# Performance work log

Measured on AMD Instinct MI355X. Metric: run time of the kernel, lower is better.

The kernel has to match this reference:

```python
import jax, jax.numpy as jnp
import numpy as np

N_CELL = 100_000
N_NET = 100_000
N_PIN = 500_000
N_NN = 200_000
N_PAIR = 500_000
RC, RN, RP = 16, 16, 8   # raw cell/net/pin feats
HC, HN, HP = 64, 64, 8   # hidden cell/net/pin feats


def _seg(x, idx, n):
    return jax.ops.segment_sum(x, idx, num_segments=n)


def _ssp(x):  # DGL ShiftedSoftplus used inside CFConv
    return jax.nn.softplus(x) - jnp.log(2.0)


def _graph_conv(x_src, src, dst, n_src, n_dst, W, b):
    # DGL GraphConv, norm='both': c_src = out_deg^-1/2, c_dst = in_deg^-1/2, degrees clamped to >=1
    ones = jnp.ones(src.shape[0], x_src.dtype)
    cs = jnp.clip(_seg(ones, src, n_src), 1.0) ** -0.5
    cd = jnp.clip(_seg(ones, dst, n_dst), 1.0) ** -0.5
    msg = _seg((x_src * cs[:, None])[src], dst, n_dst) * cd[:, None]
    return msg @ W + b


def setup_inputs() -> dict:
    key = jax.random.key(0)
    ks = jax.random.split(key, 40)
    f = lambda i, s: jax.random.normal(ks[i], s, jnp.float32)
    p = lambda i, s: jax.random.normal(ks[i], s, jnp.float32) * 0.05
    ri = lambda i, s, hi: jax.random.randint(ks[i], s, 0, hi)
    return dict(
        cell_feat=f(0, (N_CELL, RC)),
        net_feat=f(1, (N_NET, RN)),
        pin_feat=f(2, (N_PIN, RP)),
        cell_lin_w=p(3, (RC, HC)), cell_lin_b=p(4, (HC,)),
        net_lin_w=p(5, (RN, HN)), net_lin_b=p(6, (HN,)),
        pin_lin_w=p(7, (RP, HP)), pin_lin_b=p(8, (HP,)),
        pins_w=p(9, (HC, HN)), pins_b=p(10, (HN,)),
        father_w=p(11, (HN, HN)), father_b=p(12, (HN,)),
        son_w=p(13, (HN, HN)), son_b=p(14, (HN,)),
        cf_node_w=p(15, (HN, HC)), cf_node_b=p(16, (HC,)),
        cf_e1_w=p(17, (RP, HC)), cf_e1_b=p(18, (HC,)),
        cf_e2_w=p(19, (HC, HC)), cf_e2_b=p(20, (HC,)),
        cf_out_w=p(21, (HC, HC)), cf_out_b=p(22, (HC,)),
        net_dis_w=p(23, (2 * HN, 1)), net_dis_b=p(24, (1,)),
        net_angle_w=p(25, (2 * HN, 1)), net_angle_b=p(26, (1,)),
        pin_dis_w=p(27, (HC + HP + HN, 1)), pin_dis_b=p(28, (1,)),
        pin_angle_w=p(29, (HC + HP + HN, 1)), pin_angle_b=p(30, (1,)),
        pin_net=ri(31, (N_PIN,), N_NET),
        pin_cell=ri(32, (N_PIN,), N_CELL),
        nn_src=ri(33, (N_NN,), N_NET),
        nn_dst=ri(34, (N_NN,), N_NET),
        net_net_pairs=ri(35, (N_PAIR, 2), N_NET),
    )


def reference(cell_feat, net_feat, pin_feat,
              cell_lin_w, cell_lin_b, net_lin_w, net_lin_b, pin_lin_w, pin_lin_b,
              pins_w, pins_b, father_w, father_b, son_w, son_b,
              cf_node_w, cf_node_b, cf_e1_w, cf_e1_b, cf_e2_w, cf_e2_b, cf_out_w, cf_out_b,
              net_dis_w, net_dis_b, net_angle_w, net_angle_b,
              pin_dis_w, pin_dis_b, pin_angle_w, pin_angle_b,
              pin_net, pin_cell, nn_src, nn_dst, net_net_pairs):
    h_cell = jnp.tanh(cell_feat @ cell_lin_w + cell_lin_b)
    h_net = jnp.tanh(net_feat @ net_lin_w + net_lin_b)
    h_pin = jnp.tanh(pin_feat @ pin_lin_w + pin_lin_b)

    # HeteroGraphConv with aggregate='max' (all relations read the PRE-update h)
    net_pins = _graph_conv(h_cell, pin_cell, pin_net, N_CELL, N_NET, pins_w, pins_b)   # cell->net
    net_fa = _graph_conv(h_net, nn_src, nn_dst, N_NET, N_NET, father_w, father_b)      # net->net
    net_so = _graph_conv(h_net, nn_dst, nn_src, N_NET, N_NET, son_w, son_b)            # reversed
    h_net2 = jnp.maximum(jnp.maximum(net_pins, net_fa), net_so)

    # CFConv net->cell; NOTE: original passes RAW pin_feat as edge feats
    e = _ssp(_ssp(pin_feat @ cf_e1_w + cf_e1_b) @ cf_e2_w + cf_e2_b)   # [P, HC]
    hv = h_net @ cf_node_w + cf_node_b                                  # [Nn, HC]
    h_cell2 = _ssp(_seg(hv[pin_net] * e, pin_cell, N_CELL) @ cf_out_w + cf_out_b)

    # gather-based pairwise readouts
    npair = jnp.concatenate([h_net2[net_net_pairs[:, 0]], h_net2[net_net_pairs[:, 1]]], axis=-1)
    npc = jnp.concatenate([h_net2[pin_net], h_pin, h_cell2[pin_cell]], axis=-1)
    net_dis = jax.nn.softplus(npair @ net_dis_w + net_dis_b)[:, 0]
    net_angle = (npair @ net_angle_w + net_angle_b)[:, 0]
    pin_dis = jax.nn.softplus(npc @ pin_dis_w + pin_dis_b)[:, 0]
    pin_angle = (npc @ pin_angle_w + pin_angle_b)[:, 0]
    return (net_dis, net_angle, pin_dis, pin_angle)
```

## Files before the change

### kernel.cpp

```cpp
#include <hip/hip_runtime.h>
#include <math.h>

#define NCELL 100000
#define NNET  100000
#define NPIN  500000
#define NNN   200000
#define NPAIR 500000
#define NSCAN (4 * NNET)
#define SCAN_BLOCKS ((NSCAN + 1023) / 1024)
#define PART_SZ ((NNET + 7) / 8)

typedef __attribute__((ext_vector_type(8))) short short8;
typedef __attribute__((ext_vector_type(4))) float f32x4;
typedef unsigned short u16;
typedef unsigned int u32;
typedef unsigned long long u64;

__device__ __forceinline__ u16 f2bf(float x) {
    union { float f; u32 u; } v; v.f = x;
    u32 r = (v.u + 0x7FFF + ((v.u >> 16) & 1)) >> 16;
    return (u16)r;
}
__device__ __forceinline__ float bf2f(u16 u) {
    union { u32 u; float f; } v; v.u = ((u32)u) << 16; return v.f;
}
__device__ __forceinline__ u32 cvtpk(float lo, float hi) {
    u32 r;
    asm("v_cvt_pk_bf16_f32 %0, %1, %2" : "=v"(r) : "v"(lo), "v"(hi));
    return r;
}
__device__ __forceinline__ u16 f2bf_fast(float v) {
    return (u16)(cvtpk(v, v) & 0xffffu);
}
__device__ __forceinline__ float plo(u32 h) { return bf2f((u16)(h & 0xffff)); }
__device__ __forceinline__ float phi(u32 h) { return bf2f((u16)(h >> 16)); }

__device__ __forceinline__ float softplusf(float x) {
    return fmaxf(x, 0.f) + __logf(1.f + __expf(-fabsf(x)));
}
__device__ __forceinline__ float sspf(float x) {
    return softplusf(x) - 0.69314718055994530942f;
}
__device__ __forceinline__ float ftanh(float x) {
    float xc = fminf(fmaxf(x, -9.f), 9.f);
    float e = __expf(2.f * xc);
    return (e - 1.f) * __builtin_amdgcn_rcpf(e + 1.f);
}

__device__ __forceinline__ short8 load_bfrag(const float* __restrict__ W,
                                             int kt, int nt, int lane) {
    int k0 = kt * 32 + ((lane >> 4) & 3) * 8;
    int c = nt * 16 + (lane & 15);
    short8 f;
#pragma unroll
    for (int j = 0; j < 8; j++) f[j] = (short)f2bf(W[(k0 + j) * 64 + c]);
    return f;
}

__global__ void k_degrees(const int* __restrict__ pin_cell, const int* __restrict__ pin_net,
                          const int* __restrict__ nn_src, const int* __restrict__ nn_dst,
                          u32* __restrict__ cnt,
                          u32* __restrict__ rankNp, u32* __restrict__ rankC,
                          u32* __restrict__ rankD, u32* __restrict__ rankS) {
    int i = blockIdx.x * blockDim.x + threadIdx.x;
    if (i < NPIN) {
        rankNp[i] = atomicAdd(&cnt[pin_net[i]], 1u);
        rankC[i]  = atomicAdd(&cnt[NNET + pin_cell[i]], 1u);
    }
    if (i < NNN) {
        rankD[i] = atomicAdd(&cnt[2 * NNET + nn_dst[i]], 1u);
        rankS[i] = atomicAdd(&cnt[3 * NNET + nn_src[i]], 1u);
    }
}

__global__ void k_deg_fin(const u32* __restrict__ cnt, float* __restrict__ deg) {
    int i = blockIdx.x * blockDim.x + threadIdx.x;
    if (i < NSCAN) deg[i] = rsqrtf((float)max(cnt[i], 1u));
}

__global__ __launch_bounds__(256) void k_scan1(const u32* __restrict__ in,
                                               u32* __restrict__ out, u32* __restrict__ bsum) {
    __shared__ u32 sc[256];
    int t = threadIdx.x;
    int base = blockIdx.x * 1024 + t * 4;
    u32 v0 = base + 0 < NSCAN ? in[base + 0] : 0;
    u32 v1 = base + 1 < NSCAN ? in[base + 1] : 0;
    u32 v2 = base + 2 < NSCAN ? in[base + 2] : 0;
    u32 v3 = base + 3 < NSCAN ? in[base + 3] : 0;
    u32 s = v0 + v1 + v2 + v3;
    sc[t] = s; __syncthreads();
    for (int off = 1; off < 256; off <<= 1) {
        u32 x = (t >= off) ? sc[t - off] : 0; __syncthreads();
        sc[t] += x; __syncthreads();
    }
    u32 excl = sc[t] - s;
    if (base + 0 < NSCAN) out[base + 0] = excl;
    if (base + 1 < NSCAN) out[base + 1] = excl + v0;
    if (base + 2 < NSCAN) out[base + 2] = excl + v0 + v1;
    if (base + 3 < NSCAN) out[base + 3] = excl + v0 + v1 + v2;
    if (t == 255) bsum[blockIdx.x] = sc[255];
}

__global__ __launch_bounds__(512) void k_scan2(u32* __restrict__ bsum) {
    __shared__ u32 sc[512];
    int t = threadIdx.x;
    u32 v = (t < SCAN_BLOCKS) ? bsum[t] : 0;
    sc[t] = v; __syncthreads();
    for (int off = 1; off < 512; off <<= 1) {
        u32 x = (t >= off) ? sc[t - off] : 0; __syncthreads();
        sc[t] += x; __syncthreads();
    }
    if (t < SCAN_BLOCKS) bsum[t] = sc[t] - v;
}

__global__ __launch_bounds__(256) void k_scan3(u32* __restrict__ S, const u32* __restrict__ bsum) {
    int i = blockIdx.x * blockDim.x + threadIdx.x;
    if (i < NSCAN) S[i] = S[i] + bsum[i >> 10];
    if (i == 0) S[NSCAN] = 2u * NPIN + 2u * NNN;
}

__global__ __launch_bounds__(256) void k_place_part(
    const int* __restrict__ pin_cell, const int* __restrict__ pin_net,
    const int* __restrict__ nn_src, const int* __restrict__ nn_dst,
    const u32* __restrict__ S,
    const u32* __restrict__ rankNp, const u32* __restrict__ rankC,
    const u32* __restrict__ rankD, const u32* __restrict__ rankS,
    u32* __restrict__ colC, u64* __restrict__ colPN,
    u32* __restrict__ colS, u32* __restrict__ colD) {
    int part = blockIdx.x & 7;
    int grp = blockIdx.x >> 3;
    int ngrp = gridDim.x >> 3;
    int lo = part * PART_SZ, hi = lo + PART_SZ;
    int stride = ngrp * 256;
    for (int e = grp * 256 + threadIdx.x; e < NPIN; e += stride) {
        int n = pin_net[e], c = pin_cell[e];
        if (n >= lo && n < hi)
            colC[S[n] + rankNp[e]] = (u32)c;
        if (c >= lo && c < hi)
            colPN[S[NNET + c] + rankC[e] - NPIN] = (u64)(u32)e | ((u64)(u32)n << 32);
    }
    for (int i = grp * 256 + threadIdx.x; i < NNN; i += stride) {
        int s = nn_src[i], d = nn_dst[i];
        if (d >= lo && d < hi)
            colS[S[2 * NNET + d] + rankD[i] - 2u * NPIN] = (u32)s;
        if (s >= lo && s < hi)
            colD[S[3 * NNET + s] + rankS[i] - (2u * NPIN + NNN)] = (u32)d;
    }
}

__global__ __launch_bounds__(256) void k_lin16_all(
    const float* __restrict__ cf, const float* __restrict__ nf,
    const float* __restrict__ Wc, const float* __restrict__ bc,
    const float* __restrict__ Wn, const float* __restrict__ bn,
    const float* __restrict__ rC,
    u16* __restrict__ h_cell, u16* __restrict__ h_net) {
    int tid = threadIdx.x, lane = tid & 63, w = tid >> 6;
    float wc[16], wn[16];
#pragma unroll
    for (int k = 0; k < 16; k++) { wc[k] = Wc[k * 64 + lane]; wn[k] = Wn[k * 64 + lane]; }
    float bC = bc[lane], bN = bn[lane];
    int wave = blockIdx.x * 4 + w, nw = gridDim.x * 4;
    for (int r = wave; r < NCELL; r += nw) {
        const float4* ip = (const float4*)(cf + (size_t)r * 16);
        float4 a = ip[0], bv = ip[1], c = ip[2], d = ip[3];
        float acc = bC;
        acc = fmaf(a.x, wc[0], acc);  acc = fmaf(a.y, wc[1], acc);
        acc = fmaf(a.z, wc[2], acc);  acc = fmaf(a.w, wc[3], acc);
        acc = fmaf(bv.x, wc[4], acc); acc = fmaf(bv.y, wc[5], acc);
        acc = fmaf(bv.z, wc[6], acc); acc = fmaf(bv.w, wc[7], acc);
        acc = fmaf(c.x, wc[8], acc);  acc = fmaf(c.y, wc[9], acc);
        acc = fmaf(c.z, wc[10], acc); acc = fmaf(c.w, wc[11], acc);
        acc = fmaf(d.x, wc[12], acc); acc = fmaf(d.y, wc[13], acc);
        acc = fmaf(d.z, wc[14], acc); acc = fmaf(d.w, wc[15], acc);
        float v = ftanh(acc) * rC[r];
        float vp = __shfl_xor(v, 1, 64);
        if (!(lane & 1))
            *(u32*)(h_cell + (size_t)r * 64 + lane) = cvtpk(v, vp);
    }
    for (int r = wave; r < NNET; r += nw) {
        const float4* ip = (const float4*)(nf + (size_t)r * 16);
        float4 a = ip[0], bv = ip[1], c = ip[2], d = ip[3];
        float acc = bN;
        acc = fmaf(a.x, wn[0], acc);  acc = fmaf(a.y, wn[1], acc);
        acc = fmaf(a.z, wn[2], acc);  acc = fmaf(a.w, wn[3], acc);
        acc = fmaf(bv.x, wn[4], acc); acc = fmaf(bv.y, wn[5], acc);
        acc = fmaf(bv.z, wn[6], acc); acc = fmaf(bv.w, wn[7], acc);
        acc = fmaf(c.x, wn[8], acc);  acc = fmaf(c.y, wn[9], acc);
        acc = fmaf(c.z, wn[10], acc); acc = fmaf(c.w, wn[11], acc);
        acc = fmaf(d.x, wn[12], acc); acc = fmaf(d.y, wn[13], acc);
        acc = fmaf(d.z, wn[14], acc); acc = fmaf(d.w, wn[15], acc);
        float v = ftanh(acc);
        float vp = __shfl_xor(v, 1, 64);
        if (!(lane & 1))
            *(u32*)(h_net + (size_t)r * 64 + lane) = cvtpk(v, vp);
    }
}

__global__ __launch_bounds__(256) void k_gatherP(
    const u32* __restrict__ S, const u32* __restrict__ colC,
    const u16* __restrict__ h_cell, u16* __restrict__ accP) {
    int l32 = threadIdx.x & 31, off2 = l32 * 2;
    int slot = blockIdx.x * 8 + (threadIdx.x >> 5), ns = gridDim.x * 8;
    for (int n = slot; n < NNET; n += ns) {
        u32 b0 = S[n], b1 = S[n + 1];
        float fa = 0.f, fb = 0.f, ga = 0.f, gb = 0.f;
        u32 k = b0;
        for (; k + 1 < b1; k += 2) {
            u32 c0 = colC[k], c1 = colC[k + 1];
            u32 h0 = *(const u32*)(h_cell + (size_t)c0 * 64 + off2);
            u32 h1 = *(const u32*)(h_cell + (size_t)c1 * 64 + off2);
            fa += plo(h0); fb += phi(h0);
            ga += plo(h1); gb += phi(h1);
        }
        if (k < b1) {
            u32 c0 = colC[k];
            u32 h0 = *(const u32*)(h_cell + (size_t)c0 * 64 + off2);
            fa += plo(h0); fb += phi(h0);
        }
        *(u32*)(accP + (size_t)n * 64 + off2) = cvtpk(fa + ga, fb + gb);
    }
}

__global__ __launch_bounds__(256) void k_gatherFS(
    const u32* __restrict__ S, const u32* __restrict__ colS, const u32* __restrict__ colD,
    const u16* __restrict__ h_net, const float* __restrict__ rDv, const float* __restrict__ rSv,
    u16* __restrict__ accF, u16* __restrict__ accS) {
    int l32 = threadIdx.x & 31, off2 = l32 * 2;
    int slot = blockIdx.x * 8 + (threadIdx.x >> 5), ns = gridDim.x * 8;
    for (int r = slot; r < 2 * NNET; r += ns) {
        if (r < NNET) {
            int d = r;
            u32 b0 = S[2 * NNET + d] - 2u * NPIN, b1 = S[2 * NNET + d + 1] - 2u * NPIN;
            float fa = 0.f, fb = 0.f, ga = 0.f, gb = 0.f;
            u32 k = b0;
            for (; k + 1 < b1; k += 2) {
                u32 s0 = colS[k], s1 = colS[k + 1];
                float c0 = rSv[s0], c1 = rSv[s1];
                u32 h0 = *(const u32*)(h_net + (size_t)s0 * 64 + off2);
                u32 h1 = *(const u32*)(h_net + (size_t)s1 * 64 + off2);
                fa = fmaf(plo(h0), c0, fa); fb = fmaf(phi(h0), c0, fb);
                ga = fmaf(plo(h1), c1, ga); gb = fmaf(phi(h1), c1, gb);
            }
            if (k < b1) {
                u32 s0 = colS[k];
                float c0 = rSv[s0];
                u32 h0 = *(const u32*)(h_net + (size_t)s0 * 64 + off2);
                fa = fmaf(plo(h0), c0, fa); fb = fmaf(phi(h0), c0, fb);
            }
            *(u32*)(accF + (size_t)d * 64 + off2) = cvtpk(fa + ga, fb + gb);
        } else {
            int s = r - NNET;
            u32 b0 = S[3 * NNET + s] - (2u * NPIN + NNN), b1 = S[3 * NNET + s + 1] - (2u * NPIN + NNN);
            float fa = 0.f, fb = 0.f, ga = 0.f, gb = 0.f;
            u32 k = b0;
            for (; k + 1 < b1; k += 2) {
                u32 d0 = colD[k], d1 = colD[k + 1];
                float c0 = rDv[d0], c1 = rDv[d1];
                u32 h0 = *(const u32*)(h_net + (size_t)d0 * 64 + off2);
                u32 h1 = *(const u32*)(h_net + (size_t)d1 * 64 + off2);
                fa = fmaf(plo(h0), c0, fa); fb = fmaf(phi(h0), c0, fb);
                ga = fmaf(plo(h1), c1, ga); gb = fmaf(phi(h1), c1, gb);
            }
            if (k < b1) {
                u32 d0 = colD[k];
                float c0 = rDv[d0];
                u32 h0 = *(const u32*)(h_net + (size_t)d0 * 64 + off2);
                fa = fmaf(plo(h0), c0, fa); fb = fmaf(phi(h0), c0, fb);
            }
            *(u32*)(accS + (size_t)s * 64 + off2) = cvtpk(fa + ga, fb + gb);
        }
    }
}

__global__ __launch_bounds__(256) void k_gatherCell(
    const u32* __restrict__ S, const u64* __restrict__ colPN,
    const u16* __restrict__ etab, const u16* __restrict__ hv, u16* __restrict__ acc) {
    int l32 = threadIdx.x & 31, off2 = l32 * 2;
    int slot = blockIdx.x * 8 + (threadIdx.x >> 5), ns = gridDim.x * 8;
    for (int c = slot; c < NCELL; c += ns) {
        u32 b0 = S[NNET + c] - NPIN, b1 = S[NNET + c + 1] - NPIN;
        float fa = 0.f, fb = 0.f, ga = 0.f, gb = 0.f;
        u32 k = b0;
        for (; k + 1 < b1; k += 2) {
            u32 n0 = (u32)(colPN[k] >> 32), n1 = (u32)(colPN[k + 1] >> 32);
            u32 e0 = *(const u32*)(etab + (size_t)k * 64 + off2);
            u32 e1 = *(const u32*)(etab + (size_t)(k + 1) * 64 + off2);
            u32 h0 = *(const u32*)(hv + (size_t)n0 * 64 + off2);
            u32 h1 = *(const u32*)(hv + (size_t)n1 * 64 + off2);
            fa = fmaf(plo(e0), plo(h0), fa); fb = fmaf(phi(e0), phi(h0), fb);
            ga = fmaf(plo(e1), plo(h1), ga); gb = fmaf(phi(e1), phi(h1), gb);
        }
        if (k < b1) {
            u32 n0 = (u32)(colPN[k] >> 32);
            u32 e0 = *(const u32*)(etab + (size_t)k * 64 + off2);
            u32 h0 = *(const u32*)(hv + (size_t)n0 * 64 + off2);
            fa = fmaf(plo(e0), plo(h0), fa); fb = fmaf(phi(e0), phi(h0), fb);
        }
        *(u32*)(acc + (size_t)c * 64 + off2) = cvtpk(fa + ga, fb + gb);
    }
}

__global__ __launch_bounds__(256, 2) void k_combine3(
// ... 56 lines not shown
#pragma unroll
                    for (int r = 0; r < 4; r++)
                        res[nt][r] = fmaxf(res[nt][r], sa[r] * acc[r] + bias[rel][nt]);
                }
            }
        }
#pragma unroll
        for (int r = 0; r < 4; r++) {
            float a0 = 0.f, a1 = 0.f, a2 = 0.f, a3 = 0.f, a4 = 0.f, a5 = 0.f;
#pragma unroll
            for (int nt = 0; nt < 4; nt++) {
                float v = res[nt][r];
                a0 = fmaf(v, wt[0][nt], a0);
                a1 = fmaf(v, wt[1][nt], a1);
                a2 = fmaf(v, wt[2][nt], a2);
                a3 = fmaf(v, wt[3][nt], a3);
                a4 = fmaf(v, wt[4][nt], a4);
                a5 = fmaf(v, wt[5][nt], a5);
            }
#pragma unroll
            for (int off = 1; off < 16; off <<= 1) {
                a0 += __shfl_xor(a0, off, 64);
                a1 += __shfl_xor(a1, off, 64);
                a2 += __shfl_xor(a2, off, 64);
                a3 += __shfl_xor(a3, off, 64);
                a4 += __shfl_xor(a4, off, 64);
                a5 += __shfl_xor(a5, off, 64);
            }
            if (l15 == 0) {
                float* tp = ntab + (size_t)(R + g * 4 + r) * 8;
                *(float2*)tp = float2{a0, a1};
                *(float2*)(tp + 2) = float2{a2, a3};
                *(float2*)(tp + 4) = float2{a4, a5};
            }
        }
    }
}

__global__ __launch_bounds__(256, 4) void k_mm64hv(
    const u16* __restrict__ in, const float* __restrict__ W,
    const float* __restrict__ b, u16* __restrict__ out, int n) {
    int tid = threadIdx.x, lane = tid & 63, w = tid >> 6;
    int l15 = lane & 15, g = (lane >> 4) & 3;
    short8 Bf[2][4];
    float bias[4];
#pragma unroll
    for (int kt = 0; kt < 2; kt++)
#pragma unroll
        for (int nt = 0; nt < 4; nt++) Bf[kt][nt] = load_bfrag(W, kt, nt, lane);
#pragma unroll
    for (int nt = 0; nt < 4; nt++) bias[nt] = b[nt * 16 + l15];
    int wave = blockIdx.x * 4 + w, nwave = gridDim.x * 4;
    int ntile = n >> 4;
    f32x4 z = {0.f, 0.f, 0.f, 0.f};
    for (int t = wave; t < ntile; t += nwave) {
        int R = t << 4;
        const u16* rb = in + (size_t)(R + l15) * 64;
        short8 a0 = *(const short8*)(rb + g * 8);
        short8 a1 = *(const short8*)(rb + 32 + g * 8);
#pragma unroll
        for (int nt = 0; nt < 4; nt++) {
            f32x4 acc = __builtin_amdgcn_mfma_f32_16x16x32_bf16(a0, Bf[0][nt], z, 0, 0, 0);
            acc = __builtin_amdgcn_mfma_f32_16x16x32_bf16(a1, Bf[1][nt], acc, 0, 0, 0);
#pragma unroll
            for (int r = 0; r < 4; r++) {
                float v = acc[r] + bias[nt];
                float vp = __shfl_xor(v, 1, 64);
                if (!(lane & 1))
                    *(u32*)(out + (size_t)(R + g * 4 + r) * 64 + nt * 16 + l15) = cvtpk(v, vp);
            }
        }
    }
}

__global__ __launch_bounds__(256, 4) void k_emlp(
    const float* __restrict__ pin_feat, const u64* __restrict__ colPN,
    const float* __restrict__ E1, const float* __restrict__ b1,
    const float* __restrict__ E2, const float* __restrict__ b2,
    u16* __restrict__ etab) {
    __shared__ __align__(16) u16 sm[4][1024];
    int tid = threadIdx.x, lane = tid & 63, w = tid >> 6;
    int l15 = lane & 15, g = (lane >> 4) & 3;
    short8 B1[4];
#pragma unroll
    for (int nt = 0; nt < 4; nt++) {
        short8 f = {0, 0, 0, 0, 0, 0, 0, 0};
        if (lane < 16) {
            int c = nt * 16 + l15;
#pragma unroll
            for (int j = 0; j < 8; j++) f[j] = (short)f2bf(E1[j * 64 + c]);
        }
        B1[nt] = f;
    }
    short8 B2[2][4];
#pragma unroll
    for (int kt = 0; kt < 2; kt++)
#pragma unroll
        for (int nt = 0; nt < 4; nt++) B2[kt][nt] = load_bfrag(E2, kt, nt, lane);
    float bb1[4], bb2[4];
#pragma unroll
    for (int nt = 0; nt < 4; nt++) {
        bb1[nt] = b1[nt * 16 + l15];
        bb2[nt] = b2[nt * 16 + l15];
    }
    int wave = blockIdx.x * 4 + w, nwave = gridDim.x * 4;
    const int ntile = NPIN >> 4;
    f32x4 z = {0.f, 0.f, 0.f, 0.f};
    for (int t = wave; t < ntile; t += nwave) {
        int P = t << 4;
        short8 a1 = {0, 0, 0, 0, 0, 0, 0, 0};
        if (lane < 16) {
            u32 p = (u32)colPN[P + lane];
            const float4* q = (const float4*)(pin_feat + (size_t)p * 8);
            float4 u0 = q[0], u1 = q[1];
            u32 w01 = cvtpk(u0.x, u0.y), w23 = cvtpk(u0.z, u0.w);
            u32 w45 = cvtpk(u1.x, u1.y), w67 = cvtpk(u1.z, u1.w);
            a1[0] = (short)(w01 & 0xffff); a1[1] = (short)(w01 >> 16);
            a1[2] = (short)(w23 & 0xffff); a1[3] = (short)(w23 >> 16);
            a1[4] = (short)(w45 & 0xffff); a1[5] = (short)(w45 >> 16);
            a1[6] = (short)(w67 & 0xffff); a1[7] = (short)(w67 >> 16);
        }
#pragma unroll
        for (int nt = 0; nt < 4; nt++) {
            f32x4 c1 = __builtin_amdgcn_mfma_f32_16x16x32_bf16(a1, B1[nt], z, 0, 0, 0);
#pragma unroll
            for (int r = 0; r < 4; r++) {
                int row = g * 4 + r;
                int col = nt * 16 + l15;
                sm[w][row * 64 + (col ^ ((row & 7) << 3))] = f2bf_fast(sspf(c1[r] + bb1[nt]));
            }
        }
        short8 a2[2];
#pragma unroll
        for (int kt = 0; kt < 2; kt++) {
            int idx = l15 * 64 + ((kt * 32 + g * 8) ^ ((l15 & 7) << 3));
            a2[kt] = *(const short8*)&sm[w][idx];
        }
#pragma unroll
        for (int nt = 0; nt < 4; nt++) {
            f32x4 e = __builtin_amdgcn_mfma_f32_16x16x32_bf16(a2[0], B2[0][nt], z, 0, 0, 0);
            e = __builtin_amdgcn_mfma_f32_16x16x32_bf16(a2[1], B2[1][nt], e, 0, 0, 0);
#pragma unroll
            for (int r = 0; r < 4; r++) {
                float v = sspf(e[r] + bb2[nt]);
                float vp = __shfl_xor(v, 1, 64);
                if (!(lane & 1))
                    *(u32*)(etab + (size_t)(P + g * 4 + r) * 64 + nt * 16 + l15) = cvtpk(v, vp);
            }
        }
    }
}

__global__ __launch_bounds__(256, 3) void k_mm64c(
    const u16* __restrict__ in, const float* __restrict__ W, const float* __restrict__ b,
    const float* __restrict__ pdw, const float* __restrict__ paw,
    float* __restrict__ ctab, int n) {
    int tid = threadIdx.x, lane = tid & 63, w = tid >> 6;
    int l15 = lane & 15, g = (lane >> 4) & 3;
    short8 Bf[2][4];
    float bias[4], wdv[4], wav[4];
#pragma unroll
    for (int kt = 0; kt < 2; kt++)
#pragma unroll
        for (int nt = 0; nt < 4; nt++) Bf[kt][nt] = load_bfrag(W, kt, nt, lane);
#pragma unroll
    for (int nt = 0; nt < 4; nt++) {
        int c = nt * 16 + l15;
        bias[nt] = b[c];
        wdv[nt] = pdw[72 + c];
        wav[nt] = paw[72 + c];
    }
    int wave = blockIdx.x * 4 + w, nwave = gridDim.x * 4;
    int ntile = n >> 4;
    f32x4 z = {0.f, 0.f, 0.f, 0.f};
    for (int t = wave; t < ntile; t += nwave) {
        int R = t << 4;
        const u16* rb = in + (size_t)(R + l15) * 64;
        short8 a0 = *(const short8*)(rb + g * 8);
        short8 a1 = *(const short8*)(rb + 32 + g * 8);
        float sd[4] = {0.f, 0.f, 0.f, 0.f}, sa[4] = {0.f, 0.f, 0.f, 0.f};
// ... 80 lines not shown
    const float* father_w = (const float*)d_in[11];
    const float* father_b = (const float*)d_in[12];
    const float* son_w    = (const float*)d_in[13];
    const float* son_b    = (const float*)d_in[14];
    const float* cf_node_w = (const float*)d_in[15];
    const float* cf_node_b = (const float*)d_in[16];
    const float* cf_e1_w  = (const float*)d_in[17];
    const float* cf_e1_b  = (const float*)d_in[18];
    const float* cf_e2_w  = (const float*)d_in[19];
    const float* cf_e2_b  = (const float*)d_in[20];
    const float* cf_out_w = (const float*)d_in[21];
    const float* cf_out_b = (const float*)d_in[22];
    const float* net_dis_w   = (const float*)d_in[23];
    const float* net_dis_b   = (const float*)d_in[24];
    const float* net_angle_w = (const float*)d_in[25];
    const float* net_angle_b = (const float*)d_in[26];
    const float* pin_dis_w   = (const float*)d_in[27];
    const float* pin_dis_b   = (const float*)d_in[28];
    const float* pin_angle_w = (const float*)d_in[29];
    const float* pin_angle_b = (const float*)d_in[30];
    const int* pin_net = (const int*)d_in[31];
    const int* pin_cell = (const int*)d_in[32];
    const int* nn_src = (const int*)d_in[33];
    const int* nn_dst = (const int*)d_in[34];
    const int* pairs = (const int*)d_in[35];

    u16* ws16 = (u16*)d_ws;
    const size_t SZ = (size_t)NNET * 64;
    u16* h_cell   = ws16;
    u16* acc_cell = ws16;
    u16* h_net    = ws16 + SZ;
    u16* accP     = ws16 + 2 * SZ;
    u16* accF     = ws16 + 3 * SZ;
    u16* hv       = ws16 + 3 * SZ;
    u16* accS     = ws16 + 4 * SZ;
    u16* etab     = ws16 + 5 * SZ;
    u32* tail = (u32*)(ws16 + 10 * SZ);
    u32* cnt    = tail;
    u32* Sarr   = cnt + NSCAN;
    u32* rankNp = Sarr + NSCAN + 2;
    u32* rankC  = rankNp + NPIN;
    u32* rankD  = rankC + NPIN;
    u32* rankS  = rankD + NNN;
    u32* colC   = rankS + NNN;
    u32* colS   = colC + NPIN;
    u32* colD   = colS + NNN;
    u64* colPN  = (u64*)(colD + NNN);
    u32* bsum   = (u32*)(colPN + NPIN);
    float* deg  = (float*)(bsum + 512);
    float* rNp = deg;
    float* rC  = deg + NNET;
    float* rD  = deg + 2 * NNET;
    float* rS  = deg + 3 * NNET;
    float* ntab = deg + NSCAN;
    float* ctab = ntab + (size_t)NNET * 8;

    hipMemsetAsync(cnt, 0, NSCAN * sizeof(u32), stream);

    k_degrees<<<(NPIN + 255) / 256, 256, 0, stream>>>(pin_cell, pin_net, nn_src, nn_dst,
                                                      cnt, rankNp, rankC, rankD, rankS);
    k_deg_fin<<<(NSCAN + 255) / 256, 256, 0, stream>>>(cnt, deg);

    k_scan1<<<SCAN_BLOCKS, 256, 0, stream>>>(cnt, Sarr, bsum);
    k_scan2<<<1, 512, 0, stream>>>(bsum);
    k_scan3<<<(NSCAN + 255) / 256, 256, 0, stream>>>(Sarr, bsum);
    k_place_part<<<2048, 256, 0, stream>>>(pin_cell, pin_net, nn_src, nn_dst,
                                           Sarr, rankNp, rankC, rankD, rankS,
                                           colC, colPN, colS, colD);

    k_lin16_all<<<2048, 256, 0, stream>>>(cell_feat, net_feat,
                                          cell_lin_w, cell_lin_b, net_lin_w, net_lin_b,
                                          rC, h_cell, h_net);

    k_gatherP<<<2048, 256, 0, stream>>>(Sarr, colC, h_cell, accP);
    k_gatherFS<<<2048, 256, 0, stream>>>(Sarr, colS, colD, h_net, rD, rS, accF, accS);

    k_combine3<<<512, 256, 0, stream>>>(accP, pins_w, pins_b,
                                        accF, father_w, father_b,
                                        accS, son_w, son_b,
                                        rNp, rD, rS,
                                        net_dis_w, net_angle_w, pin_dis_w, pin_angle_w,
                                        ntab, NNET);

    k_mm64hv<<<1024, 256, 0, stream>>>(h_net, cf_node_w, cf_node_b, hv, NNET);

    k_emlp<<<2048, 256, 0, stream>>>(pin_feat, colPN, cf_e1_w, cf_e1_b, cf_e2_w, cf_e2_b, etab);

    k_gatherCell<<<2048, 256, 0, stream>>>(Sarr, colPN, etab, hv, acc_cell);

    k_mm64c<<<512, 256, 0, stream>>>(acc_cell, cf_out_w, cf_out_b,
                                     pin_dis_w, pin_angle_w, ctab, NCELL);

    float* out = (float*)d_out;
    k_readout<<<(NPAIR + NPIN + 255) / 256, 256, 0, stream>>>(
        pairs, pin_feat, pin_net, pin_cell, ntab, ctab,
        pin_lin_w, pin_lin_b, pin_dis_w, pin_angle_w,
        net_dis_b, net_angle_b, pin_dis_b, pin_angle_b, out);
}
```

Baseline: 310.0 us.

## Merge independent stages into block-partitioned fused kernels to cut launches

Independent stages now share one launch each, with block ranges assigning roles. Degree counting and the input linear layers run together in one kernel. The edge MLP, hv projection, pin gather and father/son gathers run together in a second kernel. The degree rsqrt moves into the scan kernel, and the rC scaling moves from the cell linear into the pin gather, since rC is not ready when the fused first kernel runs. hv gets its own workspace slot so it no longer aliases accF. The aim is fewer launches, less idle tail between stages and concurrent use of the GPU by heterogeneous work. The cost is fixed role splits that may be imbalanced and a fused kernel with higher register pressure.

```diff
diff --git a/kernel.cpp b/kernel.cpp
--- a/kernel.cpp
+++ b/kernel.cpp
@@ -10,6 +10,13 @@
 #define SCAN_BLOCKS ((NSCAN + 1023) / 1024)
 #define PART_SZ ((NNET + 7) / 8)
 
+#define GA_DEG 1024
+#define GA_LIN 1024
+#define GB_EMLP 1024
+#define GB_HV   256
+#define GB_GP   384
+#define GB_GFS  384
+
 typedef __attribute__((ext_vector_type(8))) short short8;
 typedef __attribute__((ext_vector_type(4))) float f32x4;
 typedef unsigned short u16;
@@ -57,29 +64,73 @@
     return f;
 }
 
-__global__ void k_degrees(const int* __restrict__ pin_cell, const int* __restrict__ pin_net,
-                          const int* __restrict__ nn_src, const int* __restrict__ nn_dst,
-                          u32* __restrict__ cnt,
-                          u32* __restrict__ rankNp, u32* __restrict__ rankC,
-                          u32* __restrict__ rankD, u32* __restrict__ rankS) {
-    int i = blockIdx.x * blockDim.x + threadIdx.x;
-    if (i < NPIN) {
-        rankNp[i] = atomicAdd(&cnt[pin_net[i]], 1u);
-        rankC[i]  = atomicAdd(&cnt[NNET + pin_cell[i]], 1u);
-    }
-    if (i < NNN) {
-        rankD[i] = atomicAdd(&cnt[2 * NNET + nn_dst[i]], 1u);
-        rankS[i] = atomicAdd(&cnt[3 * NNET + nn_src[i]], 1u);
-    }
-}
-
-__global__ void k_deg_fin(const u32* __restrict__ cnt, float* __restrict__ deg) {
-    int i = blockIdx.x * blockDim.x + threadIdx.x;
-    if (i < NSCAN) deg[i] = rsqrtf((float)max(cnt[i], 1u));
+__global__ __launch_bounds__(256) void k_fusedA(
+    const int* __restrict__ pin_cell, const int* __restrict__ pin_net,
+    const int* __restrict__ nn_src, const int* __restrict__ nn_dst,
+    u32* __restrict__ cnt,
+    u32* __restrict__ rankNp, u32* __restrict__ rankC,
+    u32* __restrict__ rankD, u32* __restrict__ rankS,
+    const float* __restrict__ cf, const float* __restrict__ nf,
+    const float* __restrict__ Wc, const float* __restrict__ bc,
+    const float* __restrict__ Wn, const float* __restrict__ bn,
+    u16* __restrict__ h_cell, u16* __restrict__ h_net) {
+    if (blockIdx.x < GA_DEG) {
+        int stride = GA_DEG * 256;
+        for (int i = blockIdx.x * 256 + threadIdx.x; i < NPIN; i += stride) {
+            rankNp[i] = atomicAdd(&cnt[pin_net[i]], 1u);
+            rankC[i]  = atomicAdd(&cnt[NNET + pin_cell[i]], 1u);
+        }
+        for (int i = blockIdx.x * 256 + threadIdx.x; i < NNN; i += stride) {
+            rankD[i] = atomicAdd(&cnt[2 * NNET + nn_dst[i]], 1u);
+            rankS[i] = atomicAdd(&cnt[3 * NNET + nn_src[i]], 1u);
+        }
+    } else {
+        int tid = threadIdx.x, lane = tid & 63, w = tid >> 6;
+        float wc[16], wn[16];
+#pragma unroll
+        for (int k = 0; k < 16; k++) { wc[k] = Wc[k * 64 + lane]; wn[k] = Wn[k * 64 + lane]; }
+        float bC = bc[lane], bN = bn[lane];
+        int wave = (blockIdx.x - GA_DEG) * 4 + w, nw = GA_LIN * 4;
+        for (int r = wave; r < NCELL; r += nw) {
+            const float4* ip = (const float4*)(cf + (size_t)r * 16);
+            float4 a = ip[0], bv = ip[1], c = ip[2], d = ip[3];
+            float acc = bC;
+            acc = fmaf(a.x, wc[0], acc);  acc = fmaf(a.y, wc[1], acc);
+            acc = fmaf(a.z, wc[2], acc);  acc = fmaf(a.w, wc[3], acc);
+            acc = fmaf(bv.x, wc[4], acc); acc = fmaf(bv.y, wc[5], acc);
+            acc = fmaf(bv.z, wc[6], acc); acc = fmaf(bv.w, wc[7], acc);
+            acc = fmaf(c.x, wc[8], acc);  acc = fmaf(c.y, wc[9], acc);
+            acc = fmaf(c.z, wc[10], acc); acc = fmaf(c.w, wc[11], acc);
+            acc = fmaf(d.x, wc[12], acc); acc = fmaf(d.y, wc[13], acc);
+            acc = fmaf(d.z, wc[14], acc); acc = fmaf(d.w, wc[15], acc);
+            float v = ftanh(acc);
+            float vp = __shfl_xor(v, 1, 64);
+            if (!(lane & 1))
+                *(u32*)(h_cell + (size_t)r * 64 + lane) = cvtpk(v, vp);
+        }
+        for (int r = wave; r < NNET; r += nw) {
+            const float4* ip = (const float4*)(nf + (size_t)r * 16);
+            float4 a = ip[0], bv = ip[1], c = ip[2], d = ip[3];
+            float acc = bN;
+            acc = fmaf(a.x, wn[0], acc);  acc = fmaf(a.y, wn[1], acc);
+            acc = fmaf(a.z, wn[2], acc);  acc = fmaf(a.w, wn[3], acc);
+            acc = fmaf(bv.x, wn[4], acc); acc = fmaf(bv.y, wn[5], acc);
+            acc = fmaf(bv.z, wn[6], acc); acc = fmaf(bv.w, wn[7], acc);
+            acc = fmaf(c.x, wn[8], acc);  acc = fmaf(c.y, wn[9], acc);
+            acc = fmaf(c.z, wn[10], acc); acc = fmaf(c.w, wn[11], acc);
+            acc = fmaf(d.x, wn[12], acc); acc = fmaf(d.y, wn[13], acc);
+            acc = fmaf(d.z, wn[14], acc); acc = fmaf(d.w, wn[15], acc);
+            float v = ftanh(acc);
+            float vp = __shfl_xor(v, 1, 64);
+            if (!(lane & 1))
+                *(u32*)(h_net + (size_t)r * 64 + lane) = cvtpk(v, vp);
+        }
+    }
 }
 
 __global__ __launch_bounds__(256) void k_scan1(const u32* __restrict__ in,
-                                               u32* __restrict__ out, u32* __restrict__ bsum) {
+                                               u32* __restrict__ out, u32* __restrict__ bsum,
+                                               float* __restrict__ deg) {
     __shared__ u32 sc[256];
     int t = threadIdx.x;
     int base = blockIdx.x * 1024 + t * 4;
@@ -87,6 +138,10 @@
     u32 v1 = base + 1 < NSCAN ? in[base + 1] : 0;
     u32 v2 = base + 2 < NSCAN ? in[base + 2] : 0;
     u32 v3 = base + 3 < NSCAN ? in[base + 3] : 0;
+    if (base + 0 < NSCAN) deg[base + 0] = rsqrtf((float)max(v0, 1u));
+    if (base + 1 < NSCAN) deg[base + 1] = rsqrtf((float)max(v1, 1u));
+    if (base + 2 < NSCAN) deg[base + 2] = rsqrtf((float)max(v2, 1u));
+    if (base + 3 < NSCAN) deg[base + 3] = rsqrtf((float)max(v3, 1u));
     u32 s = v0 + v1 + v2 + v3;
     sc[t] = s; __syncthreads();
     for (int off = 1; off < 256; off <<= 1) {
@@ -148,126 +203,188 @@
     }
 }
 
-__global__ __launch_bounds__(256) void k_lin16_all(
-    const float* __restrict__ cf, const float* __restrict__ nf,
-    const float* __restrict__ Wc, const float* __restrict__ bc,
-    const float* __restrict__ Wn, const float* __restrict__ bn,
-    const float* __restrict__ rC,
-    u16* __restrict__ h_cell, u16* __restrict__ h_net) {
+__global__ __launch_bounds__(256, 4) void k_fusedB(
+    const float* __restrict__ pin_feat, const u64* __restrict__ colPN,
+    const float* __restrict__ E1, const float* __restrict__ b1,
+    const float* __restrict__ E2, const float* __restrict__ b2,
+    u16* __restrict__ etab,
+    const u16* __restrict__ h_net, const float* __restrict__ Whv,
+    const float* __restrict__ bhv, u16* __restrict__ hv,
+    const u32* __restrict__ S, const u32* __restrict__ colC,
+    const u16* __restrict__ h_cell, const float* __restrict__ rCv,
+    u16* __restrict__ accP,
+    const u32* __restrict__ colS, const u32* __restrict__ colD,
+    const float* __restrict__ rDv, const float* __restrict__ rSv,
+    u16* __restrict__ accF, u16* __restrict__ accS) {
+    __shared__ __align__(16) u16 sm[4][1024];
     int tid = threadIdx.x, lane = tid & 63, w = tid >> 6;
-    float wc[16], wn[16];
-#pragma unroll
-    for (int k = 0; k < 16; k++) { wc[k] = Wc[k * 64 + lane]; wn[k] = Wn[k * 64 + lane]; }
-    float bC = bc[lane], bN = bn[lane];
-    int wave = blockIdx.x * 4 + w, nw = gridDim.x * 4;
-    for (int r = wave; r < NCELL; r += nw) {
-        const float4* ip = (const float4*)(cf + (size_t)r * 16);
-        float4 a = ip[0], bv = ip[1], c = ip[2], d = ip[3];
-        float acc = bC;
-        acc = fmaf(a.x, wc[0], acc);  acc = fmaf(a.y, wc[1], acc);
-        acc = fmaf(a.z, wc[2], acc);  acc = fmaf(a.w, wc[3], acc);
-        acc = fmaf(bv.x, wc[4], acc); acc = fmaf(bv.y, wc[5], acc);
-        acc = fmaf(bv.z, wc[6], acc); acc = fmaf(bv.w, wc[7], acc);
-        acc = fmaf(c.x, wc[8], acc);  acc = fmaf(c.y, wc[9], acc);
-        acc = fmaf(c.z, wc[10], acc); acc = fmaf(c.w, wc[11], acc);
-        acc = fmaf(d.x, wc[12], acc); acc = fmaf(d.y, wc[13], acc);
-        acc = fmaf(d.z, wc[14], acc); acc = fmaf(d.w, wc[15], acc);
-        float v = ftanh(acc) * rC[r];
-        float vp = __shfl_xor(v, 1, 64);
-        if (!(lane & 1))
-            *(u32*)(h_cell + (size_t)r * 64 + lane) = cvtpk(v, vp);
-    }
-    for (int r = wave; r < NNET; r += nw) {
-        const float4* ip = (const float4*)(nf + (size_t)r * 16);
-        float4 a = ip[0], bv = ip[1], c = ip[2], d = ip[3];
-        float acc = bN;
-        acc = fmaf(a.x, wn[0], acc);  acc = fmaf(a.y, wn[1], acc);
-        acc = fmaf(a.z, wn[2], acc);  acc = fmaf(a.w, wn[3], acc);
-        acc = fmaf(bv.x, wn[4], acc); acc = fmaf(bv.y, wn[5], acc);
-        acc = fmaf(bv.z, wn[6], acc); acc = fmaf(bv.w, wn[7], acc);
-        acc = fmaf(c.x, wn[8], acc);  acc = fmaf(c.y, wn[9], acc);
-        acc = fmaf(c.z, wn[10], acc); acc = fmaf(c.w, wn[11], acc);
-        acc = fmaf(d.x, wn[12], acc); acc = fmaf(d.y, wn[13], acc);
-        acc = fmaf(d.z, wn[14], acc); acc = fmaf(d.w, wn[15], acc);
-        float v = ftanh(acc);
-        float vp = __shfl_xor(v, 1, 64);
-        if (!(lane & 1))
-            *(u32*)(h_net + (size_t)r * 64 + lane) = cvtpk(v, vp);
-    }
-}
-
-__global__ __launch_bounds__(256) void k_gatherP(
-    const u32* __restrict__ S, const u32* __restrict__ colC,
-    const u16* __restrict__ h_cell, u16* __restrict__ accP) {
-    int l32 = threadIdx.x & 31, off2 = l32 * 2;
-    int slot = blockIdx.x * 8 + (threadIdx.x >> 5), ns = gridDim.x * 8;
-    for (int n = slot; n < NNET; n += ns) {
-        u32 b0 = S[n], b1 = S[n + 1];
-        float fa = 0.f, fb = 0.f, ga = 0.f, gb = 0.f;
-        u32 k = b0;
-        for (; k + 1 < b1; k += 2) {
-            u32 c0 = colC[k], c1 = colC[k + 1];
-            u32 h0 = *(const u32*)(h_cell + (size_t)c0 * 64 + off2);
-            u32 h1 = *(const u32*)(h_cell + (size_t)c1 * 64 + off2);
-            fa += plo(h0); fb += phi(h0);
-            ga += plo(h1); gb += phi(h1);
-        }
-        if (k < b1) {
-            u32 c0 = colC[k];
-            u32 h0 = *(const u32*)(h_cell + (size_t)c0 * 64 + off2);
-            fa += plo(h0); fb += phi(h0);
-        }
-        *(u32*)(accP + (size_t)n * 64 + off2) = cvtpk(fa + ga, fb + gb);
-    }
-}
-
-__global__ __launch_bounds__(256) void k_gatherFS(
-    const u32* __restrict__ S, const u32* __restrict__ colS, const u32* __restrict__ colD,
-    const u16* __restrict__ h_net, const float* __restrict__ rDv, const float* __restrict__ rSv,
-    u16* __restrict__ accF, u16* __restrict__ accS) {
-    int l32 = threadIdx.x & 31, off2 = l32 * 2;
-    int slot = blockIdx.x * 8 + (threadIdx.x >> 5), ns = gridDim.x * 8;
-    for (int r = slot; r < 2 * NNET; r += ns) {
-        if (r < NNET) {
-            int d = r;
-            u32 b0 = S[2 * NNET + d] - 2u * NPIN, b1 = S[2 * NNET + d + 1] - 2u * NPIN;
+    int l15 = lane & 15, g = (lane >> 4) & 3;
+    f32x4 z = {0.f, 0.f, 0.f, 0.f};
+    if (blockIdx.x < GB_EMLP) {
+        short8 B1[4];
+#pragma unroll
+        for (int nt = 0; nt < 4; nt++) {
+            short8 f = {0, 0, 0, 0, 0, 0, 0, 0};
+            if (lane < 16) {
+                int c = nt * 16 + l15;
+#pragma unroll
+                for (int j = 0; j < 8; j++) f[j] = (short)f2bf(E1[j * 64 + c]);
+            }
+            B1[nt] = f;
+        }
+        short8 B2[2][4];
+#pragma unroll
+        for (int kt = 0; kt < 2; kt++)
+#pragma unroll
+            for (int nt = 0; nt < 4; nt++) B2[kt][nt] = load_bfrag(E2, kt, nt, lane);
+        float bb1[4], bb2[4];
+#pragma unroll
+        for (int nt = 0; nt < 4; nt++) {
+            bb1[nt] = b1[nt * 16 + l15];
+            bb2[nt] = b2[nt * 16 + l15];
+        }
+        int wave = blockIdx.x * 4 + w, nwave = GB_EMLP * 4;
+        const int ntile = NPIN >> 4;
+        for (int t = wave; t < ntile; t += nwave) {
+            int P = t << 4;
+            short8 a1 = {0, 0, 0, 0, 0, 0, 0, 0};
+            if (lane < 16) {
+                u32 p = (u32)colPN[P + lane];
+                const float4* q = (const float4*)(pin_feat + (size_t)p * 8);
+                float4 u0 = q[0], u1 = q[1];
+                u32 w01 = cvtpk(u0.x, u0.y), w23 = cvtpk(u0.z, u0.w);
+                u32 w45 = cvtpk(u1.x, u1.y), w67 = cvtpk(u1.z, u1.w);
+                a1[0] = (short)(w01 & 0xffff); a1[1] = (short)(w01 >> 16);
+                a1[2] = (short)(w23 & 0xffff); a1[3] = (short)(w23 >> 16);
+                a1[4] = (short)(w45 & 0xffff); a1[5] = (short)(w45 >> 16);
+                a1[6] = (short)(w67 & 0xffff); a1[7] = (short)(w67 >> 16);
+            }
+#pragma unroll
+            for (int nt = 0; nt < 4; nt++) {
+                f32x4 c1 = __builtin_amdgcn_mfma_f32_16x16x32_bf16(a1, B1[nt], z, 0, 0, 0);
+#pragma unroll
+                for (int r = 0; r < 4; r++) {
+                    int row = g * 4 + r;
+                    int col = nt * 16 + l15;
+                    sm[w][row * 64 + (col ^ ((row & 7) << 3))] = f2bf_fast(sspf(c1[r] + bb1[nt]));
+                }
+            }
+            short8 a2[2];
+#pragma unroll
+            for (int kt = 0; kt < 2; kt++) {
+                int idx = l15 * 64 + ((kt * 32 + g * 8) ^ ((l15 & 7) << 3));
+                a2[kt] = *(const short8*)&sm[w][idx];
+            }
+#pragma unroll
+            for (int nt = 0; nt < 4; nt++) {
+                f32x4 e = __builtin_amdgcn_mfma_f32_16x16x32_bf16(a2[0], B2[0][nt], z, 0, 0, 0);
+                e = __builtin_amdgcn_mfma_f32_16x16x32_bf16(a2[1], B2[1][nt], e, 0, 0, 0);
+#pragma unroll
+                for (int r = 0; r < 4; r++) {
+                    float v = sspf(e[r] + bb2[nt]);
+                    float vp = __shfl_xor(v, 1, 64);
+                    if (!(lane & 1))
+                        *(u32*)(etab + (size_t)(P + g * 4 + r) * 64 + nt * 16 + l15) = cvtpk(v, vp);
+                }
+            }
+        }
+    } else if (blockIdx.x < GB_EMLP + GB_HV) {
+        short8 Bf[2][4];
+        float bias[4];
+#pragma unroll
+        for (int kt = 0; kt < 2; kt++)
+#pragma unroll
+            for (int nt = 0; nt < 4; nt++) Bf[kt][nt] = load_bfrag(Whv, kt, nt, lane);
+#pragma unroll
+        for (int nt = 0; nt < 4; nt++) bias[nt] = bhv[nt * 16 + l15];
+        int wave = (blockIdx.x - GB_EMLP) * 4 + w, nwave = GB_HV * 4;
+        int ntile = NNET >> 4;
+        for (int t = wave; t < ntile; t += nwave) {
+            int R = t << 4;
+            const u16* rb = h_net + (size_t)(R + l15) * 64;
+            short8 a0 = *(const short8*)(rb + g * 8);
+            short8 a1 = *(const short8*)(rb + 32 + g * 8);
+#pragma unroll
+            for (int nt = 0; nt < 4; nt++) {
+                f32x4 acc = __builtin_amdgcn_mfma_f32_16x16x32_bf16(a0, Bf[0][nt], z, 0, 0, 0);
+                acc = __builtin_amdgcn_mfma_f32_16x16x32_bf16(a1, Bf[1][nt], acc, 0, 0, 0);
+#pragma unroll
+                for (int r = 0; r < 4; r++) {
+                    float v = acc[r] + bias[nt];
+                    float vp = __shfl_xor(v, 1, 64);
+                    if (!(lane & 1))
+                        *(u32*)(hv + (size_t)(R + g * 4 + r) * 64 + nt * 16 + l15) = cvtpk(v, vp);
+                }
+            }
+        }
+    } else if (blockIdx.x < GB_EMLP + GB_HV + GB_GP) {
+        int l32 = tid & 31, off2 = l32 * 2;
+        int slot = (blockIdx.x - GB_EMLP - GB_HV) * 8 + (tid >> 5), ns = GB_GP * 8;
+        for (int n = slot; n < NNET; n += ns) {
+            u32 b0 = S[n], b1 = S[n + 1];
             float fa = 0.f, fb = 0.f, ga = 0.f, gb = 0.f;
             u32 k = b0;
             for (; k + 1 < b1; k += 2) {
-                u32 s0 = colS[k], s1 = colS[k + 1];
-                float c0 = rSv[s0], c1 = rSv[s1];
-                u32 h0 = *(const u32*)(h_net + (size_t)s0 * 64 + off2);
-                u32 h1 = *(const u32*)(h_net + (size_t)s1 * 64 + off2);
-                fa = fmaf(plo(h0), c0, fa); fb = fmaf(phi(h0), c0, fb);
-                ga = fmaf(plo(h1), c1, ga); gb = fmaf(phi(h1), c1, gb);
+                u32 c0 = colC[k], c1 = colC[k + 1];
+                float r0 = rCv[c0], r1 = rCv[c1];
+                u32 h0 = *(const u32*)(h_cell + (size_t)c0 * 64 + off2);
+                u32 h1 = *(const u32*)(h_cell + (size_t)c1 * 64 + off2);
+                fa = fmaf(plo(h0), r0, fa); fb = fmaf(phi(h0), r0, fb);
+                ga = fmaf(plo(h1), r1, ga); gb = fmaf(phi(h1), r1, gb);
             }
             if (k < b1) {
-                u32 s0 = colS[k];
-                float c0 = rSv[s0];
-                u32 h0 = *(const u32*)(h_net + (size_t)s0 * 64 + off2);
-                fa = fmaf(plo(h0), c0, fa); fb = fmaf(phi(h0), c0, fb);
-            }
-            *(u32*)(accF + (size_t)d * 64 + off2) = cvtpk(fa + ga, fb + gb);
-        } else {
-            int s = r - NNET;
-            u32 b0 = S[3 * NNET + s] - (2u * NPIN + NNN), b1 = S[3 * NNET + s + 1] - (2u * NPIN + NNN);
-            float fa = 0.f, fb = 0.f, ga = 0.f, gb = 0.f;
-            u32 k = b0;
-            for (; k + 1 < b1; k += 2) {
-                u32 d0 = colD[k], d1 = colD[k + 1];
-                float c0 = rDv[d0], c1 = rDv[d1];
-                u32 h0 = *(const u32*)(h_net + (size_t)d0 * 64 + off2);
-                u32 h1 = *(const u32*)(h_net + (size_t)d1 * 64 + off2);
-                fa = fmaf(plo(h0), c0, fa); fb = fmaf(phi(h0), c0, fb);
-                ga = fmaf(plo(h1), c1, ga); gb = fmaf(phi(h1), c1, gb);
-            }
-            if (k < b1) {
-                u32 d0 = colD[k];
-                float c0 = rDv[d0];
-                u32 h0 = *(const u32*)(h_net + (size_t)d0 * 64 + off2);
-                fa = fmaf(plo(h0), c0, fa); fb = fmaf(phi(h0), c0, fb);
-            }
-            *(u32*)(accS + (size_t)s * 64 + off2) = cvtpk(fa + ga, fb + gb);
+                u32 c0 = colC[k];
+                float r0 = rCv[c0];
+                u32 h0 = *(const u32*)(h_cell + (size_t)c0 * 64 + off2);
+                fa = fmaf(plo(h0), r0, fa); fb = fmaf(phi(h0), r0, fb);
+            }
+            *(u32*)(accP + (size_t)n * 64 + off2) = cvtpk(fa + ga, fb + gb);
+        }
+    } else {
+        int l32 = tid & 31, off2 = l32 * 2;
+        int slot = (blockIdx.x - GB_EMLP - GB_HV - GB_GP) * 8 + (tid >> 5), ns = GB_GFS * 8;
+        for (int r = slot; r < 2 * NNET; r += ns) {
+            if (r < NNET) {
+                int d = r;
+                u32 b0 = S[2 * NNET + d] - 2u * NPIN, b1 = S[2 * NNET + d + 1] - 2u * NPIN;
+                float fa = 0.f, fb = 0.f, ga = 0.f, gb = 0.f;
+                u32 k = b0;
+                for (; k + 1 < b1; k += 2) {
+                    u32 s0 = colS[k], s1 = colS[k + 1];
+                    float c0 = rSv[s0], c1 = rSv[s1];
+                    u32 h0 = *(const u32*)(h_net + (size_t)s0 * 64 + off2);
+                    u32 h1 = *(const u32*)(h_net + (size_t)s1 * 64 + off2);
+                    fa = fmaf(plo(h0), c0, fa); fb = fmaf(phi(h0), c0, fb);
+                    ga = fmaf(plo(h1), c1, ga); gb = fmaf(phi(h1), c1, gb);
+                }
+                if (k < b1) {
+                    u32 s0 = colS[k];
+                    float c0 = rSv[s0];
+                    u32 h0 = *(const u32*)(h_net + (size_t)s0 * 64 + off2);
+                    fa = fmaf(plo(h0), c0, fa); fb = fmaf(phi(h0), c0, fb);
+                }
+                *(u32*)(accF + (size_t)d * 64 + off2) = cvtpk(fa + ga, fb + gb);
+            } else {
+                int s = r - NNET;
+                u32 b0 = S[3 * NNET + s] - (2u * NPIN + NNN), b1 = S[3 * NNET + s + 1] - (2u * NPIN + NNN);
+                float fa = 0.f, fb = 0.f, ga = 0.f, gb = 0.f;
+                u32 k = b0;
+                for (; k + 1 < b1; k += 2) {
+                    u32 d0 = colD[k], d1 = colD[k + 1];
+                    float c0 = rDv[d0], c1 = rDv[d1];
+                    u32 h0 = *(const u32*)(h_net + (size_t)d0 * 64 + off2);
+                    u32 h1 = *(const u32*)(h_net + (size_t)d1 * 64 + off2);
+                    fa = fmaf(plo(h0), c0, fa); fb = fmaf(phi(h0), c0, fb);
+                    ga = fmaf(plo(h1), c1, ga); gb = fmaf(phi(h1), c1, gb);
+                }
+                if (k < b1) {
+                    u32 d0 = colD[k];
+                    float c0 = rDv[d0];
+                    u32 h0 = *(const u32*)(h_net + (size_t)d0 * 64 + off2);
+                    fa = fmaf(plo(h0), c0, fa); fb = fmaf(phi(h0), c0, fb);
+                }
+                *(u32*)(accS + (size_t)s * 64 + off2) = cvtpk(fa + ga, fb + gb);
+            }
         }
     }
 }
@@ -390,120 +507,6 @@
                 *(float2*)tp = float2{a0, a1};
                 *(float2*)(tp + 2) = float2{a2, a3};
                 *(float2*)(tp + 4) = float2{a4, a5};
-            }
-        }
-    }
-}
-
-__global__ __launch_bounds__(256, 4) void k_mm64hv(
-    const u16* __restrict__ in, const float* __restrict__ W,
-    const float* __restrict__ b, u16* __restrict__ out, int n) {
-    int tid = threadIdx.x, lane = tid & 63, w = tid >> 6;
-    int l15 = lane & 15, g = (lane >> 4) & 3;
-    short8 Bf[2][4];
-    float bias[4];
-#pragma unroll
-    for (int kt = 0; kt < 2; kt++)
-#pragma unroll
-        for (int nt = 0; nt < 4; nt++) Bf[kt][nt] = load_bfrag(W, kt, nt, lane);
-#pragma unroll
-    for (int nt = 0; nt < 4; nt++) bias[nt] = b[nt * 16 + l15];
-    int wave = blockIdx.x * 4 + w, nwave = gridDim.x * 4;
-    int ntile = n >> 4;
-    f32x4 z = {0.f, 0.f, 0.f, 0.f};
-    for (int t = wave; t < ntile; t += nwave) {
-        int R = t << 4;
-        const u16* rb = in + (size_t)(R + l15) * 64;
-        short8 a0 = *(const short8*)(rb + g * 8);
-        short8 a1 = *(const short8*)(rb + 32 + g * 8);
-#pragma unroll
-        for (int nt = 0; nt < 4; nt++) {
-            f32x4 acc = __builtin_amdgcn_mfma_f32_16x16x32_bf16(a0, Bf[0][nt], z, 0, 0, 0);
-            acc = __builtin_amdgcn_mfma_f32_16x16x32_bf16(a1, Bf[1][nt], acc, 0, 0, 0);
-#pragma unroll
-            for (int r = 0; r < 4; r++) {
-                float v = acc[r] + bias[nt];
-                float vp = __shfl_xor(v, 1, 64);
-                if (!(lane & 1))
-                    *(u32*)(out + (size_t)(R + g * 4 + r) * 64 + nt * 16 + l15) = cvtpk(v, vp);
-            }
-        }
-    }
-}
-
-__global__ __launch_bounds__(256, 4) void k_emlp(
-    const float* __restrict__ pin_feat, const u64* __restrict__ colPN,
-    const float* __restrict__ E1, const float* __restrict__ b1,
-    const float* __restrict__ E2, const float* __restrict__ b2,
-    u16* __restrict__ etab) {
-    __shared__ __align__(16) u16 sm[4][1024];
-    int tid = threadIdx.x, lane = tid & 63, w = tid >> 6;
-    int l15 = lane & 15, g = (lane >> 4) & 3;
-    short8 B1[4];
-#pragma unroll
-    for (int nt = 0; nt < 4; nt++) {
-        short8 f = {0, 0, 0, 0, 0, 0, 0, 0};
-        if (lane < 16) {
-            int c = nt * 16 + l15;
-#pragma unroll
-            for (int j = 0; j < 8; j++) f[j] = (short)f2bf(E1[j * 64 + c]);
-        }
-        B1[nt] = f;
-    }
-    short8 B2[2][4];
-#pragma unroll
-    for (int kt = 0; kt < 2; kt++)
-#pragma unroll
-        for (int nt = 0; nt < 4; nt++) B2[kt][nt] = load_bfrag(E2, kt, nt, lane);
-    float bb1[4], bb2[4];
-#pragma unroll
-    for (int nt = 0; nt < 4; nt++) {
-        bb1[nt] = b1[nt * 16 + l15];
-        bb2[nt] = b2[nt * 16 + l15];
-    }
-    int wave = blockIdx.x * 4 + w, nwave = gridDim.x * 4;
-    const int ntile = NPIN >> 4;
-    f32x4 z = {0.f, 0.f, 0.f, 0.f};
-    for (int t = wave; t < ntile; t += nwave) {
-        int P = t << 4;
-        short8 a1 = {0, 0, 0, 0, 0, 0, 0, 0};
-        if (lane < 16) {
-            u32 p = (u32)colPN[P + lane];
-            const float4* q = (const float4*)(pin_feat + (size_t)p * 8);
-            float4 u0 = q[0], u1 = q[1];
-            u32 w01 = cvtpk(u0.x, u0.y), w23 = cvtpk(u0.z, u0.w);
-            u32 w45 = cvtpk(u1.x, u1.y), w67 = cvtpk(u1.z, u1.w);
-            a1[0] = (short)(w01 & 0xffff); a1[1] = (short)(w01 >> 16);
-            a1[2] = (short)(w23 & 0xffff); a1[3] = (short)(w23 >> 16);
-            a1[4] = (short)(w45 & 0xffff); a1[5] = (short)(w45 >> 16);
-            a1[6] = (short)(w67 & 0xffff); a1[7] = (short)(w67 >> 16);
-        }
-#pragma unroll
-        for (int nt = 0; nt < 4; nt++) {
-            f32x4 c1 = __builtin_amdgcn_mfma_f32_16x16x32_bf16(a1, B1[nt], z, 0, 0, 0);
-#pragma unroll
-            for (int r = 0; r < 4; r++) {
-                int row = g * 4 + r;
-                int col = nt * 16 + l15;
-                sm[w][row * 64 + (col ^ ((row & 7) << 3))] = f2bf_fast(sspf(c1[r] + bb1[nt]));
-            }
-        }
-        short8 a2[2];
-#pragma unroll
-        for (int kt = 0; kt < 2; kt++) {
-            int idx = l15 * 64 + ((kt * 32 + g * 8) ^ ((l15 & 7) << 3));
-            a2[kt] = *(const short8*)&sm[w][idx];
-        }
-#pragma unroll
-        for (int nt = 0; nt < 4; nt++) {
-            f32x4 e = __builtin_amdgcn_mfma_f32_16x16x32_bf16(a2[0], B2[0][nt], z, 0, 0, 0);
-            e = __builtin_amdgcn_mfma_f32_16x16x32_bf16(a2[1], B2[1][nt], e, 0, 0, 0);
-#pragma unroll
-            for (int r = 0; r < 4; r++) {
-                float v = sspf(e[r] + bb2[nt]);
-                float vp = __shfl_xor(v, 1, 64);
-                if (!(lane & 1))
-                    *(u32*)(etab + (size_t)(P + g * 4 + r) * 64 + nt * 16 + l15) = cvtpk(v, vp);
             }
         }
     }
@@ -650,10 +653,10 @@
     u16* h_net    = ws16 + SZ;
     u16* accP     = ws16 + 2 * SZ;
     u16* accF     = ws16 + 3 * SZ;
-    u16* hv       = ws16 + 3 * SZ;
     u16* accS     = ws16 + 4 * SZ;
     u16* etab     = ws16 + 5 * SZ;
-    u32* tail = (u32*)(ws16 + 10 * SZ);
+    u16* hv       = ws16 + 10 * SZ;
+    u32* tail = (u32*)(ws16 + 11 * SZ);
     u32* cnt    = tail;
     u32* Sarr   = cnt + NSCAN;
     u32* rankNp = Sarr + NSCAN + 2;
@@ -675,23 +678,23 @@
 
     hipMemsetAsync(cnt, 0, NSCAN * sizeof(u32), stream);
 
-    k_degrees<<<(NPIN + 255) / 256, 256, 0, stream>>>(pin_cell, pin_net, nn_src, nn_dst,
-                                                      cnt, rankNp, rankC, rankD, rankS);
-    k_deg_fin<<<(NSCAN + 255) / 256, 256, 0, stream>>>(cnt, deg);
-
-    k_scan1<<<SCAN_BLOCKS, 256, 0, stream>>>(cnt, Sarr, bsum);
+    k_fusedA<<<GA_DEG + GA_LIN, 256, 0, stream>>>(
+        pin_cell, pin_net, nn_src, nn_dst, cnt, rankNp, rankC, rankD, rankS,
+        cell_feat, net_feat, cell_lin_w, cell_lin_b, net_lin_w, net_lin_b,
+        h_cell, h_net);
+
+    k_scan1<<<SCAN_BLOCKS, 256, 0, stream>>>(cnt, Sarr, bsum, deg);
     k_scan2<<<1, 512, 0, stream>>>(bsum);
     k_scan3<<<(NSCAN + 255) / 256, 256, 0, stream>>>(Sarr, bsum);
     k_place_part<<<2048, 256, 0, stream>>>(pin_cell, pin_net, nn_src, nn_dst,
                                            Sarr, rankNp, rankC, rankD, rankS,
                                            colC, colPN, colS, colD);
 
-    k_lin16_all<<<2048, 256, 0, stream>>>(cell_feat, net_feat,
-                                          cell_lin_w, cell_lin_b, net_lin_w, net_lin_b,
-                                          rC, h_cell, h_net);
-
-    k_gatherP<<<2048, 256, 0, stream>>>(Sarr, colC, h_cell, accP);
-    k_gatherFS<<<2048, 256, 0, stream>>>(Sarr, colS, colD, h_net, rD, rS, accF, accS);
+    k_fusedB<<<GB_EMLP + GB_HV + GB_GP + GB_GFS, 256, 0, stream>>>(
+        pin_feat, colPN, cf_e1_w, cf_e1_b, cf_e2_w, cf_e2_b, etab,
+        h_net, cf_node_w, cf_node_b, hv,
+        Sarr, colC, h_cell, rC, accP,
+        colS, colD, rD, rS, accF, accS);
 
     k_combine3<<<512, 256, 0, stream>>>(accP, pins_w, pins_b,
                                         accF, father_w, father_b,
@@ -700,10 +703,6 @@
                                         net_dis_w, net_angle_w, pin_dis_w, pin_angle_w,
                                         ntab, NNET);
 
-    k_mm64hv<<<1024, 256, 0, stream>>>(h_net, cf_node_w, cf_node_b, hv, NNET);
-
-    k_emlp<<<2048, 256, 0, stream>>>(pin_feat, colPN, cf_e1_w, cf_e1_b, cf_e2_w, cf_e2_b, etab);
-
     k_gatherCell<<<2048, 256, 0, stream>>>(Sarr, colPN, etab, hv, acc_cell);
 
     k_mm64c<<<512, 256, 0, stream>>>(acc_cell, cf_out_w, cf_out_b,
```

New measurement: 341.4 us. 1.1x slower.
